# Kernel optimization log

Measured on AMD Instinct MI355X. Metric: run time of the kernel, lower is better.

The kernel has to match this reference:

```python
import jax, jax.numpy as jnp
import numpy as np

N = 1024        # hidden_size
M = 16000       # output_size (vocab)
T = 50          # encoder sequence length
NP = 50         # max_length (attention proj dim n_prime)


def setup_inputs() -> dict:
    key = jax.random.key(0)
    ks = jax.random.split(key, 24)
    f32 = jnp.float32
    def rnd(k, shape):
        return jax.random.normal(k, shape, dtype=f32) * 0.02
    inp = {
        'output': jax.random.normal(ks[0], (M, 1), dtype=f32),
        'hidden': jax.random.normal(ks[1], (N, 1), dtype=f32),
        'encoder_outputs': jax.random.normal(ks[2], (T, 2 * N), dtype=f32),
        # decoder GRU-like weights
        'W':  rnd(ks[3], (M, N)),
        'Wz': rnd(ks[4], (M, N)),
        'Wr': rnd(ks[5], (M, N)),
        'Wo': rnd(ks[6], (M, 2 * N)),
        'U':  rnd(ks[7], (N, N)),
        'Uz': rnd(ks[8], (N, N)),
        'Ur': rnd(ks[9], (N, N)),
        'Uo': rnd(ks[10], (4 * N, N)),
        'C':  rnd(ks[11], (2 * N, N)),
        'Cz': rnd(ks[12], (2 * N, N)),
        'Cr': rnd(ks[13], (2 * N, N)),
        'Co': rnd(ks[14], (4 * N, 2 * N)),
        'Vo': rnd(ks[15], (4 * N, M)),
        # attention weights
        'Va': rnd(ks[16], (NP, 1)),
        'Wa': rnd(ks[17], (NP, N)),
        'Ua': rnd(ks[18], (NP, 2 * N)),
    }
    return inp


def reference(output, hidden, encoder_outputs, W, Wz, Wr, Wo, U, Uz, Ur, Uo,
              C, Cz, Cr, Co, Vo, Va, Wa, Ua):
    y, s, h = output, hidden, encoder_outputs  # (M,1), (N,1), (T,2N)
    # --- Bahdanau attention (vectorized version of get_c's python loop) ---
    # e_i = exp(Va^T tanh(Wa@s + Ua@h_i)); then normalized -> softmax
    scores = jnp.tanh((Wa @ s).T + h @ Ua.T) @ Va          # (T,1)
    attn = jax.nn.softmax(scores[:, 0])                     # (T,)
    alpha = h * attn[:, None]                               # (T,2N) weighted enc outputs
    c = jnp.sum(alpha, axis=0)[:, None]                     # (2N,1) context
    # --- GRU-like decoder step (note: s_tilde uses sigmoid, per source) ---
    r = jax.nn.sigmoid(Wr.T @ y + Ur.T @ s + Cr.T @ c)      # (N,1)
    z = jax.nn.sigmoid(Wz.T @ y + Uz.T @ s + Cz.T @ c)      # (N,1)
    s_tilde = jax.nn.sigmoid(W.T @ y + U.T @ (r * s) + C.T @ c)
    s_new = (1.0 - z) * s + z * s_tilde                     # (N,1)
    # --- maxout output layer ---
    t_tilde = jax.nn.sigmoid(Uo @ s_new + Vo @ y + Co @ c)  # (4N,1)
    t = jnp.max(t_tilde.reshape(-1, 2, 1), axis=1)          # (2N,1) pairwise max
    logits = Wo @ t                                         # (M,1)
    log_sm = jax.nn.log_softmax(logits, axis=0)             # log(softmax(., dim=0))
    # dropout in the source is applied to a discarded value -> mathematical no-op
    return (log_sm, s_new, alpha)
```

## Files before the change

kernel.cpp:

```cpp
#include <hip/hip_runtime.h>
#include <math.h>

#define DEV_INLINE __device__ __forceinline__

DEV_INLINE float sigmoidf_(float x) { return 1.0f / (1.0f + expf(-x)); }

DEV_INLINE float wave_reduce(float v) {
#pragma unroll
    for (int off = 32; off; off >>= 1) v += __shfl_down(v, off, 64);
    return v;
}

DEV_INLINE float wave_dotN(const float* __restrict__ row, const float* __restrict__ x,
                           int nv, int lane) {
    const float4* r4 = (const float4*)row;
    const float4* x4 = (const float4*)x;
    float a0 = 0.f, a1 = 0.f, a2 = 0.f, a3 = 0.f;
    int i = lane;
    for (; i + 192 < nv; i += 256) {
        float4 p0 = r4[i],       q0 = x4[i];
        float4 p1 = r4[i + 64],  q1 = x4[i + 64];
        float4 p2 = r4[i + 128], q2 = x4[i + 128];
        float4 p3 = r4[i + 192], q3 = x4[i + 192];
        a0 = fmaf(p0.x, q0.x, fmaf(p0.y, q0.y, fmaf(p0.z, q0.z, fmaf(p0.w, q0.w, a0))));
        a1 = fmaf(p1.x, q1.x, fmaf(p1.y, q1.y, fmaf(p1.z, q1.z, fmaf(p1.w, q1.w, a1))));
        a2 = fmaf(p2.x, q2.x, fmaf(p2.y, q2.y, fmaf(p2.z, q2.z, fmaf(p2.w, q2.w, a2))));
        a3 = fmaf(p3.x, q3.x, fmaf(p3.y, q3.y, fmaf(p3.z, q3.z, fmaf(p3.w, q3.w, a3))));
    }
    for (; i < nv; i += 64) {
        float4 p = r4[i], q = x4[i];
        a0 = fmaf(p.x, q.x, fmaf(p.y, q.y, fmaf(p.z, q.z, fmaf(p.w, q.w, a0))));
    }
    return wave_reduce(a0 + a1 + a2 + a3);
}

DEV_INLINE void colgemv_block(const float* __restrict__ A, const float* __restrict__ x,
                              float* __restrict__ out, int r0, int r1) {
    int c4 = threadIdx.x;
    const float4* A4 = (const float4*)A;
    float4 s0 = make_float4(0.f, 0.f, 0.f, 0.f);
    float4 s1 = make_float4(0.f, 0.f, 0.f, 0.f);
    int r = r0;
    for (; r + 8 <= r1; r += 8) {
        float4 av[8];
        float xs[8];
#pragma unroll
        for (int k = 0; k < 8; ++k) av[k] = A4[(size_t)(r + k) * 256 + c4];
#pragma unroll
        for (int k = 0; k < 8; ++k) xs[k] = x[r + k];
#pragma unroll
        for (int k = 0; k < 8; ++k) {
            float4 a = av[k];
            float xv = xs[k];
            if (k & 1) {
                s1.x = fmaf(xv, a.x, s1.x); s1.y = fmaf(xv, a.y, s1.y);
                s1.z = fmaf(xv, a.z, s1.z); s1.w = fmaf(xv, a.w, s1.w);
            } else {
                s0.x = fmaf(xv, a.x, s0.x); s0.y = fmaf(xv, a.y, s0.y);
                s0.z = fmaf(xv, a.z, s0.z); s0.w = fmaf(xv, a.w, s0.w);
            }
        }
    }
    for (; r < r1; ++r) {
        float xv = x[r];
        float4 a = A4[(size_t)r * 256 + c4];
        s0.x = fmaf(xv, a.x, s0.x); s0.y = fmaf(xv, a.y, s0.y);
        s0.z = fmaf(xv, a.z, s0.z); s0.w = fmaf(xv, a.w, s0.w);
    }
    int c = c4 * 4;
    atomicAdd(out + c + 0, s0.x + s1.x);
    atomicAdd(out + c + 1, s0.y + s1.y);
    atomicAdd(out + c + 2, s0.z + s1.z);
    atomicAdd(out + c + 3, s0.w + s1.w);
}

__global__ void k_scores(const float* __restrict__ Wa, const float* __restrict__ Ua,
                         const float* __restrict__ h, const float* __restrict__ s,
                         float* __restrict__ em) {
    int i = blockIdx.x;
    int w = threadIdx.x >> 6, lane = threadIdx.x & 63;
    for (int j = w; j < 50; j += 4) {
        float d1 = wave_dotN(Wa + j * 1024, s, 256, lane);
        float d2 = wave_dotN(Ua + j * 2048, h + i * 2048, 512, lane);
        if (lane == 0) em[i * 50 + j] = tanhf(d1 + d2);
    }
}

__global__ void k_alpha_c(const float* __restrict__ h, const float* __restrict__ Va,
                          const float* __restrict__ em, float* __restrict__ cvec,
                          float* __restrict__ alpha_out) {
    __shared__ float attn_s[50];
    int tid = threadIdx.x;
    if (tid < 64) {
        float sc = -1e30f;
        if (tid < 50) {
            float t = 0.f;
            for (int j = 0; j < 50; ++j) t = fmaf(Va[j], em[tid * 50 + j], t);
            sc = t;
        }
        float m = sc;
#pragma unroll
        for (int off = 32; off; off >>= 1) m = fmaxf(m, __shfl_xor(m, off, 64));
        float e = (tid < 50) ? expf(sc - m) : 0.f;
        float ssum = e;
#pragma unroll
        for (int off = 32; off; off >>= 1) ssum += __shfl_xor(ssum, off, 64);
        if (tid < 50) attn_s[tid] = e / ssum;
    }
    __syncthreads();
    int g = blockIdx.x * 256 + tid;
    float csum = 0.f;
    for (int i = 0; i < 50; ++i) {
        float a = h[i * 2048 + g] * attn_s[i];
        alpha_out[i * 2048 + g] = a;
        csum += a;
    }
    cvec[g] = csum;
}

__global__ void k_megaA(const float* __restrict__ W, const float* __restrict__ Wz,
                        const float* __restrict__ Wr, const float* __restrict__ Uz,
                        const float* __restrict__ Ur, const float* __restrict__ C,
                        const float* __restrict__ Cz, const float* __restrict__ Cr,
                        const float* __restrict__ Vo, const float* __restrict__ Co,
                        const float* __restrict__ y, const float* __restrict__ s,
                        const float* __restrict__ cvec, float* acc_r, float* acc_z,
                        float* acc_st, float* acc_t) {
    int b = blockIdx.x;
    if (b < 128) { colgemv_block(W, y, acc_st, b * 125, b * 125 + 125); return; }
    b -= 128;
    if (b < 128) { colgemv_block(Wz, y, acc_z, b * 125, b * 125 + 125); return; }
    b -= 128;
    if (b < 128) { colgemv_block(Wr, y, acc_r, b * 125, b * 125 + 125); return; }
    b -= 128;
    if (b < 8) { colgemv_block(Uz, s, acc_z, b * 128, b * 128 + 128); return; }
    b -= 8;
    if (b < 8) { colgemv_block(Ur, s, acc_r, b * 128, b * 128 + 128); return; }
    b -= 8;
    if (b < 16) { colgemv_block(C, cvec, acc_st, b * 128, b * 128 + 128); return; }
    b -= 16;
    if (b < 16) { colgemv_block(Cz, cvec, acc_z, b * 128, b * 128 + 128); return; }
    b -= 16;
    if (b < 16) { colgemv_block(Cr, cvec, acc_r, b * 128, b * 128 + 128); return; }
    b -= 16;
    {
        int wid = (b * 256 + threadIdx.x) >> 6;
        int lane = threadIdx.x & 63;
        float v1 = wave_dotN(Vo + (size_t)wid * 16000, y, 4000, lane);
        float v2 = wave_dotN(Co + (size_t)wid * 2048, cvec, 512, lane);
        if (lane == 0) acc_t[wid] = v1 + v2;
    }
}

__global__ void k_rzUst(const float* __restrict__ U, const float* __restrict__ acc_r,
                        const float* __restrict__ s, float* acc_st) {
    __shared__ float rs_s[1024];
    int tid = threadIdx.x;
#pragma unroll
    for (int k = 0; k < 4; ++k) {
        int n = tid + 256 * k;
        rs_s[n] = sigmoidf_(acc_r[n]) * s[n];
    }
    __syncthreads();
    colgemv_block(U, rs_s, acc_st, blockIdx.x * 128, blockIdx.x * 128 + 128);
}

__global__ void k_uoco_snew(const float* __restrict__ Uo, const float* __restrict__ acc_st,
                            const float* __restrict__ acc_z, const float* __restrict__ s,
                            float* __restrict__ acc_t, float* __restrict__ out_snew) {
    __shared__ float sn[1024];
    int tid = threadIdx.x;
#pragma unroll
    for (int k = 0; k < 4; ++k) {
        int n = tid + 256 * k;
        float z = sigmoidf_(acc_z[n]);
        float st = sigmoidf_(acc_st[n]);
        float v = (1.f - z) * s[n] + z * st;
        sn[n] = v;
        if (blockIdx.x == 0) out_snew[n] = v;
    }
    __syncthreads();
    int w = tid >> 6, lane = tid & 63;
#pragma unroll
    for (int k = 0; k < 4; ++k) {
        int row = blockIdx.x * 16 + w * 4 + k;
        float d = wave_dotN(Uo + (size_t)row * 1024, sn, 256, lane);
        if (lane == 0) acc_t[row] += d;
    }
}

__global__ void k_tmax(const float* __restrict__ acc_t, float* __restrict__ tvec) {
    int k = blockIdx.x * 256 + threadIdx.x;
    tvec[k] = fmaxf(sigmoidf_(acc_t[2 * k]), sigmoidf_(acc_t[2 * k + 1]));
}

__global__ void k_wo(const float* __restrict__ Wo, const float* __restrict__ tvec,
                     float* __restrict__ logits) {
    int wid = (blockIdx.x * 256 + threadIdx.x) >> 6;
    int lane = threadIdx.x & 63;
    float v = wave_dotN(Wo + (size_t)wid * 2048, tvec, 512, lane);
    if (lane == 0) logits[wid] = v;
}

__global__ void k_logsm(float* __restrict__ out) {
    __shared__ float red[16];
    __shared__ float bval;
    int tid = threadIdx.x, lane = tid & 63, w = tid >> 6;
    float m = -1e30f;
    for (int i = tid; i < 16000; i += 1024) m = fmaxf(m, out[i]);
#pragma unroll
    for (int off = 32; off; off >>= 1) m = fmaxf(m, __shfl_xor(m, off, 64));
    if (lane == 0) red[w] = m;
    __syncthreads();
    if (tid == 0) {
        float mm = red[0];
        for (int i = 1; i < 16; ++i) mm = fmaxf(mm, red[i]);
        bval = mm;
    }
    __syncthreads();
    float M = bval;
    float sum = 0.f;
    for (int i = tid; i < 16000; i += 1024) sum += expf(out[i] - M);
#pragma unroll
    for (int off = 32; off; off >>= 1) sum += __shfl_xor(sum, off, 64);
    if (lane == 0) red[w] = sum;
    __syncthreads();
    if (tid == 0) {
        float ss = 0.f;
        for (int i = 0; i < 16; ++i) ss += red[i];
        bval = M + logf(ss);
    }
    __syncthreads();
    float lse = bval;
    for (int i = tid; i < 16000; i += 1024) out[i] -= lse;
}

extern "C" void kernel_launch(void* const* d_in, const int* in_sizes, int n_in,
                              void* d_out, int out_size, void* d_ws, size_t ws_size,
                              hipStream_t stream) {
    const float* y  = (const float*)d_in[0];
    const float* s  = (const float*)d_in[1];
    const float* h  = (const float*)d_in[2];
    const float* W  = (const float*)d_in[3];
    const float* Wz = (const float*)d_in[4];
    const float* Wr = (const float*)d_in[5];
    const float* Wo = (const float*)d_in[6];
    const float* U  = (const float*)d_in[7];
    const float* Uz = (const float*)d_in[8];
    const float* Ur = (const float*)d_in[9];
    const float* Uo = (const float*)d_in[10];
    const float* C  = (const float*)d_in[11];
    const float* Cz = (const float*)d_in[12];
    const float* Cr = (const float*)d_in[13];
    const float* Co = (const float*)d_in[14];
    const float* Vo = (const float*)d_in[15];
    const float* Va = (const float*)d_in[16];
    const float* Wa = (const float*)d_in[17];
    const float* Ua = (const float*)d_in[18];

    float* out = (float*)d_out;
    float* ws  = (float*)d_ws;

    float* acc_r  = ws;
    float* acc_z  = ws + 1024;
    float* acc_st = ws + 2048;
    float* acc_t  = ws + 3072;
    float* em     = ws + 7168;
    float* cvec   = ws + 9728;
    float* tvec   = ws + 11776;

    hipMemsetAsync(ws, 0, 3072 * sizeof(float), stream);
    k_scores<<<50, 256, 0, stream>>>(Wa, Ua, h, s, em);
    k_alpha_c<<<8, 256, 0, stream>>>(h, Va, em, cvec, out + 17024);
    k_megaA<<<1472, 256, 0, stream>>>(W, Wz, Wr, Uz, Ur, C, Cz, Cr, Vo, Co,
                                      y, s, cvec, acc_r, acc_z, acc_st, acc_t);
    k_rzUst<<<8, 256, 0, stream>>>(U, acc_r, s, acc_st);
    k_uoco_snew<<<256, 256, 0, stream>>>(Uo, acc_st, acc_z, s, acc_t, out + 16000);
    k_tmax<<<8, 256, 0, stream>>>(acc_t, tvec);
    k_wo<<<4000, 256, 0, stream>>>(Wo, tvec, out);
    k_logsm<<<1, 1024, 0, stream>>>(out);
}
```

Measured before the change: 685.5 us.

## Fuse all decoder stages into one persistent kernel with atomic flag dependencies

Replaces the eight kernel launches with a single 1835-block kernel in which block ranges play each stage and use global atomic counters to wait for their producer stages. Independent work such as the Vo/W/Wz/Wr GEMVs can overlap the attention and later stages, and launch gaps and the separate tmax and logsoftmax kernels go away; the maxout is folded into the Uo stage and log-softmax is vectorized. The cost is spin-waiting blocks occupying CUs. Correctness relies on blocks being scheduled in roughly ascending order, so there is a deadlock risk if consumers become resident before producers.

After: 1.133 ms. 65.3% more time.

```diff
diff --git a/kernel.cpp b/kernel.cpp
--- a/kernel.cpp
+++ b/kernel.cpp
@@ -74,165 +74,203 @@
     atomicAdd(out + c + 3, s0.w + s1.w);
 }
 
-__global__ void k_scores(const float* __restrict__ Wa, const float* __restrict__ Ua,
-                         const float* __restrict__ h, const float* __restrict__ s,
-                         float* __restrict__ em) {
-    int i = blockIdx.x;
-    int w = threadIdx.x >> 6, lane = threadIdx.x & 63;
-    for (int j = w; j < 50; j += 4) {
-        float d1 = wave_dotN(Wa + j * 1024, s, 256, lane);
-        float d2 = wave_dotN(Ua + j * 2048, h + i * 2048, 512, lane);
-        if (lane == 0) em[i * 50 + j] = tanhf(d1 + d2);
-    }
-}
-
-__global__ void k_alpha_c(const float* __restrict__ h, const float* __restrict__ Va,
-                          const float* __restrict__ em, float* __restrict__ cvec,
-                          float* __restrict__ alpha_out) {
-    __shared__ float attn_s[50];
-    int tid = threadIdx.x;
-    if (tid < 64) {
-        float sc = -1e30f;
-        if (tid < 50) {
-            float t = 0.f;
-            for (int j = 0; j < 50; ++j) t = fmaf(Va[j], em[tid * 50 + j], t);
-            sc = t;
-        }
-        float m = sc;
+DEV_INLINE void signal_flag(int* f) {
+    __threadfence();
+    __syncthreads();
+    if (threadIdx.x == 0) atomicAdd(f, 1);
+}
+DEV_INLINE void wait_flag(int* f, int target) {
+    if (threadIdx.x == 0) {
+        while (atomicAdd(f, 0) < target) __builtin_amdgcn_s_sleep(127);
+    }
+    __syncthreads();
+    __threadfence();
+}
+
+__global__ __launch_bounds__(256, 8) void k_fused(
+    const float* __restrict__ y, const float* __restrict__ s, const float* __restrict__ h,
+    const float* __restrict__ W, const float* __restrict__ Wz, const float* __restrict__ Wr,
+    const float* __restrict__ Wo, const float* __restrict__ U, const float* __restrict__ Uz,
+    const float* __restrict__ Ur, const float* __restrict__ Uo, const float* __restrict__ C,
+    const float* __restrict__ Cz, const float* __restrict__ Cr, const float* __restrict__ Co,
+    const float* __restrict__ Vo, const float* __restrict__ Va, const float* __restrict__ Wa,
+    const float* __restrict__ Ua, float* __restrict__ out, float* __restrict__ ws)
+{
+    float* acc_r  = ws;
+    float* acc_z  = ws + 1024;
+    float* acc_st = ws + 2048;
+    float* acc_t  = ws + 3072;
+    int*   flags  = (int*)(ws + 7168);
+    float* em     = ws + 7296;
+    float* cvec   = ws + 9856;
+    float* tvec   = ws + 11904;
+    int* fSC  = flags;
+    int* fAL  = flags + 16;
+    int* fR   = flags + 32;
+    int* fMID = flags + 48;
+    int* fU   = flags + 64;
+    int* fWO  = flags + 80;
+
+    __shared__ float sm[1024];
+    __shared__ float sred[8];
+    __shared__ float sbval;
+
+    const int bid  = blockIdx.x;
+    const int tid  = threadIdx.x;
+    const int w    = tid >> 6;
+    const int lane = tid & 63;
+
+    if (bid < 50) {
+        int i = bid;
+        for (int j = w; j < 50; j += 4) {
+            float d1 = wave_dotN(Wa + j * 1024, s, 256, lane);
+            float d2 = wave_dotN(Ua + j * 2048, h + i * 2048, 512, lane);
+            if (lane == 0) em[i * 50 + j] = tanhf(d1 + d2);
+        }
+        signal_flag(fSC);
+        return;
+    }
+    if (bid < 58) {
+        wait_flag(fSC, 50);
+        if (tid < 64) {
+            float sc = -1e30f;
+            if (tid < 50) {
+                float t = 0.f;
+                for (int j = 0; j < 50; ++j) t = fmaf(Va[j], em[tid * 50 + j], t);
+                sc = t;
+            }
+            float m = sc;
+#pragma unroll
+            for (int off = 32; off; off >>= 1) m = fmaxf(m, __shfl_xor(m, off, 64));
+            float e = (tid < 50) ? expf(sc - m) : 0.f;
+            float ssum = e;
+#pragma unroll
+            for (int off = 32; off; off >>= 1) ssum += __shfl_xor(ssum, off, 64);
+            if (tid < 50) sm[tid] = e / ssum;
+        }
+        __syncthreads();
+        int g = (bid - 50) * 256 + tid;
+        float csum = 0.f;
+        float* alpha_out = out + 17024;
+        for (int i2 = 0; i2 < 50; ++i2) {
+            float a = h[i2 * 2048 + g] * sm[i2];
+            alpha_out[i2 * 2048 + g] = a;
+            csum += a;
+        }
+        cvec[g] = csum;
+        signal_flag(fAL);
+        return;
+    }
+    if (bid < 186) { int b = bid - 58;  colgemv_block(W,  y, acc_st, b * 125, b * 125 + 125); signal_flag(fMID); return; }
+    if (bid < 314) { int b = bid - 186; colgemv_block(Wz, y, acc_z,  b * 125, b * 125 + 125); signal_flag(fMID); return; }
+    if (bid < 442) { int b = bid - 314; colgemv_block(Wr, y, acc_r,  b * 125, b * 125 + 125); signal_flag(fR);   return; }
+    if (bid < 450) { int b = bid - 442; colgemv_block(Uz, s, acc_z,  b * 128, b * 128 + 128); signal_flag(fMID); return; }
+    if (bid < 458) { int b = bid - 450; colgemv_block(Ur, s, acc_r,  b * 128, b * 128 + 128); signal_flag(fR);   return; }
+    if (bid < 474) { int b = bid - 458; wait_flag(fAL, 8); colgemv_block(C,  cvec, acc_st, b * 128, b * 128 + 128); signal_flag(fMID); return; }
+    if (bid < 490) { int b = bid - 474; wait_flag(fAL, 8); colgemv_block(Cz, cvec, acc_z,  b * 128, b * 128 + 128); signal_flag(fMID); return; }
+    if (bid < 506) { int b = bid - 490; wait_flag(fAL, 8); colgemv_block(Cr, cvec, acc_r,  b * 128, b * 128 + 128); signal_flag(fR);   return; }
+    if (bid < 522) {
+        int b = bid - 506;
+        wait_flag(fR, 152);
+#pragma unroll
+        for (int k = 0; k < 4; ++k) {
+            int n = tid + 256 * k;
+            sm[n] = sigmoidf_(acc_r[n]) * s[n];
+        }
+        __syncthreads();
+        colgemv_block(U, sm, acc_st, b * 64, b * 64 + 64);
+        signal_flag(fMID);
+        return;
+    }
+    if (bid < 778) {
+        int b = bid - 522;
+        int row0 = b * 16 + w * 4;
+        float v1[4];
+#pragma unroll
+        for (int k = 0; k < 4; ++k)
+            v1[k] = wave_dotN(Vo + (size_t)(row0 + k) * 16000, y, 4000, lane);
+        wait_flag(fAL, 8);
+#pragma unroll
+        for (int k = 0; k < 4; ++k) {
+            float v2 = wave_dotN(Co + (size_t)(row0 + k) * 2048, cvec, 512, lane);
+            if (lane == 0) atomicAdd(acc_t + row0 + k, v1[k] + v2);
+        }
+        signal_flag(fMID);
+        return;
+    }
+    if (bid < 1034) {
+        int b = bid - 778;
+        wait_flag(fMID, 568);
+#pragma unroll
+        for (int k = 0; k < 4; ++k) {
+            int n = tid + 256 * k;
+            float z  = sigmoidf_(acc_z[n]);
+            float st = sigmoidf_(acc_st[n]);
+            float v = (1.f - z) * s[n] + z * st;
+            sm[n] = v;
+            if (b == 0) out[16000 + n] = v;
+        }
+        __syncthreads();
+        float m0 = 0.f;
+#pragma unroll
+        for (int k = 0; k < 4; ++k) {
+            int row = b * 16 + w * 4 + k;
+            float d = wave_dotN(Uo + (size_t)row * 1024, sm, 256, lane);
+            if (lane == 0) {
+                float tf = sigmoidf_(acc_t[row] + d);
+                if (k & 1) tvec[row >> 1] = fmaxf(m0, tf);
+                else       m0 = tf;
+            }
+        }
+        signal_flag(fU);
+        return;
+    }
+    if (bid < 1834) {
+        int b = bid - 1034;
+        wait_flag(fU, 256);
+        int gw = b * 4 + w;
+#pragma unroll
+        for (int k = 0; k < 5; ++k) {
+            int row = gw * 5 + k;
+            float v = wave_dotN(Wo + (size_t)row * 2048, tvec, 512, lane);
+            if (lane == 0) out[row] = v;
+        }
+        signal_flag(fWO);
+        return;
+    }
+    wait_flag(fWO, 800);
+    {
+        float4* o4 = (float4*)out;
+        float m = -1e30f;
+        for (int i = tid; i < 4000; i += 256) {
+            float4 v = o4[i];
+            m = fmaxf(m, fmaxf(fmaxf(v.x, v.y), fmaxf(v.z, v.w)));
+        }
 #pragma unroll
         for (int off = 32; off; off >>= 1) m = fmaxf(m, __shfl_xor(m, off, 64));
-        float e = (tid < 50) ? expf(sc - m) : 0.f;
-        float ssum = e;
-#pragma unroll
-        for (int off = 32; off; off >>= 1) ssum += __shfl_xor(ssum, off, 64);
-        if (tid < 50) attn_s[tid] = e / ssum;
-    }
-    __syncthreads();
-    int g = blockIdx.x * 256 + tid;
-    float csum = 0.f;
-    for (int i = 0; i < 50; ++i) {
-        float a = h[i * 2048 + g] * attn_s[i];
-        alpha_out[i * 2048 + g] = a;
-        csum += a;
-    }
-    cvec[g] = csum;
-}
-
-__global__ void k_megaA(const float* __restrict__ W, const float* __restrict__ Wz,
-                        const float* __restrict__ Wr, const float* __restrict__ Uz,
-                        const float* __restrict__ Ur, const float* __restrict__ C,
-                        const float* __restrict__ Cz, const float* __restrict__ Cr,
-                        const float* __restrict__ Vo, const float* __restrict__ Co,
-                        const float* __restrict__ y, const float* __restrict__ s,
-                        const float* __restrict__ cvec, float* acc_r, float* acc_z,
-                        float* acc_st, float* acc_t) {
-    int b = blockIdx.x;
-    if (b < 128) { colgemv_block(W, y, acc_st, b * 125, b * 125 + 125); return; }
-    b -= 128;
-    if (b < 128) { colgemv_block(Wz, y, acc_z, b * 125, b * 125 + 125); return; }
-    b -= 128;
-    if (b < 128) { colgemv_block(Wr, y, acc_r, b * 125, b * 125 + 125); return; }
-    b -= 128;
-    if (b < 8) { colgemv_block(Uz, s, acc_z, b * 128, b * 128 + 128); return; }
-    b -= 8;
-    if (b < 8) { colgemv_block(Ur, s, acc_r, b * 128, b * 128 + 128); return; }
-    b -= 8;
-    if (b < 16) { colgemv_block(C, cvec, acc_st, b * 128, b * 128 + 128); return; }
-    b -= 16;
-    if (b < 16) { colgemv_block(Cz, cvec, acc_z, b * 128, b * 128 + 128); return; }
-    b -= 16;
-    if (b < 16) { colgemv_block(Cr, cvec, acc_r, b * 128, b * 128 + 128); return; }
-    b -= 16;
-    {
-        int wid = (b * 256 + threadIdx.x) >> 6;
-        int lane = threadIdx.x & 63;
-        float v1 = wave_dotN(Vo + (size_t)wid * 16000, y, 4000, lane);
-        float v2 = wave_dotN(Co + (size_t)wid * 2048, cvec, 512, lane);
-        if (lane == 0) acc_t[wid] = v1 + v2;
-    }
-}
-
-__global__ void k_rzUst(const float* __restrict__ U, const float* __restrict__ acc_r,
-                        const float* __restrict__ s, float* acc_st) {
-    __shared__ float rs_s[1024];
-    int tid = threadIdx.x;
-#pragma unroll
-    for (int k = 0; k < 4; ++k) {
-        int n = tid + 256 * k;
-        rs_s[n] = sigmoidf_(acc_r[n]) * s[n];
-    }
-    __syncthreads();
-    colgemv_block(U, rs_s, acc_st, blockIdx.x * 128, blockIdx.x * 128 + 128);
-}
-
-__global__ void k_uoco_snew(const float* __restrict__ Uo, const float* __restrict__ acc_st,
-                            const float* __restrict__ acc_z, const float* __restrict__ s,
-                            float* __restrict__ acc_t, float* __restrict__ out_snew) {
-    __shared__ float sn[1024];
-    int tid = threadIdx.x;
-#pragma unroll
-    for (int k = 0; k < 4; ++k) {
-        int n = tid + 256 * k;
-        float z = sigmoidf_(acc_z[n]);
-        float st = sigmoidf_(acc_st[n]);
-        float v = (1.f - z) * s[n] + z * st;
-        sn[n] = v;
-        if (blockIdx.x == 0) out_snew[n] = v;
-    }
-    __syncthreads();
-    int w = tid >> 6, lane = tid & 63;
-#pragma unroll
-    for (int k = 0; k < 4; ++k) {
-        int row = blockIdx.x * 16 + w * 4 + k;
-        float d = wave_dotN(Uo + (size_t)row * 1024, sn, 256, lane);
-        if (lane == 0) acc_t[row] += d;
-    }
-}
-
-__global__ void k_tmax(const float* __restrict__ acc_t, float* __restrict__ tvec) {
-    int k = blockIdx.x * 256 + threadIdx.x;
-    tvec[k] = fmaxf(sigmoidf_(acc_t[2 * k]), sigmoidf_(acc_t[2 * k + 1]));
-}
-
-__global__ void k_wo(const float* __restrict__ Wo, const float* __restrict__ tvec,
-                     float* __restrict__ logits) {
-    int wid = (blockIdx.x * 256 + threadIdx.x) >> 6;
-    int lane = threadIdx.x & 63;
-    float v = wave_dotN(Wo + (size_t)wid * 2048, tvec, 512, lane);
-    if (lane == 0) logits[wid] = v;
-}
-
-__global__ void k_logsm(float* __restrict__ out) {
-    __shared__ float red[16];
-    __shared__ float bval;
-    int tid = threadIdx.x, lane = tid & 63, w = tid >> 6;
-    float m = -1e30f;
-    for (int i = tid; i < 16000; i += 1024) m = fmaxf(m, out[i]);
-#pragma unroll
-    for (int off = 32; off; off >>= 1) m = fmaxf(m, __shfl_xor(m, off, 64));
-    if (lane == 0) red[w] = m;
-    __syncthreads();
-    if (tid == 0) {
-        float mm = red[0];
-        for (int i = 1; i < 16; ++i) mm = fmaxf(mm, red[i]);
-        bval = mm;
-    }
-    __syncthreads();
-    float M = bval;
-    float sum = 0.f;
-    for (int i = tid; i < 16000; i += 1024) sum += expf(out[i] - M);
-#pragma unroll
-    for (int off = 32; off; off >>= 1) sum += __shfl_xor(sum, off, 64);
-    if (lane == 0) red[w] = sum;
-    __syncthreads();
-    if (tid == 0) {
-        float ss = 0.f;
-        for (int i = 0; i < 16; ++i) ss += red[i];
-        bval = M + logf(ss);
-    }
-    __syncthreads();
-    float lse = bval;
-    for (int i = tid; i < 16000; i += 1024) out[i] -= lse;
+        if (lane == 0) sred[w] = m;
+        __syncthreads();
+        if (tid == 0) sbval = fmaxf(fmaxf(sred[0], sred[1]), fmaxf(sred[2], sred[3]));
+        __syncthreads();
+        float M = sbval;
+        float sum = 0.f;
+        for (int i = tid; i < 4000; i += 256) {
+            float4 v = o4[i];
+            sum += expf(v.x - M) + expf(v.y - M) + expf(v.z - M) + expf(v.w - M);
+        }
+#pragma unroll
+        for (int off = 32; off; off >>= 1) sum += __shfl_xor(sum, off, 64);
+        if (lane == 0) sred[w] = sum;
+        __syncthreads();
+        if (tid == 0) sbval = M + logf(sred[0] + sred[1] + sred[2] + sred[3]);
+        __syncthreads();
+        float lse = sbval;
+        for (int i = tid; i < 4000; i += 256) {
+            float4 v = o4[i];
+            v.x -= lse; v.y -= lse; v.z -= lse; v.w -= lse;
+            o4[i] = v;
+        }
+    }
 }
 
 extern "C" void kernel_launch(void* const* d_in, const int* in_sizes, int n_in,
@@ -261,22 +299,7 @@
     float* out = (float*)d_out;
     float* ws  = (float*)d_ws;
 
-    float* acc_r  = ws;
-    float* acc_z  = ws + 1024;
-    float* acc_st = ws + 2048;
-    float* acc_t  = ws + 3072;
-    float* em     = ws + 7168;
-    float* cvec   = ws + 9728;
-    float* tvec   = ws + 11776;
-
-    hipMemsetAsync(ws, 0, 3072 * sizeof(float), stream);
-    k_scores<<<50, 256, 0, stream>>>(Wa, Ua, h, s, em);
-    k_alpha_c<<<8, 256, 0, stream>>>(h, Va, em, cvec, out + 17024);
-    k_megaA<<<1472, 256, 0, stream>>>(W, Wz, Wr, Uz, Ur, C, Cz, Cr, Vo, Co,
-                                      y, s, cvec, acc_r, acc_z, acc_st, acc_t);
-    k_rzUst<<<8, 256, 0, stream>>>(U, acc_r, s, acc_st);
-    k_uoco_snew<<<256, 256, 0, stream>>>(Uo, acc_st, acc_z, s, acc_t, out + 16000);
-    k_tmax<<<8, 256, 0, stream>>>(acc_t, tvec);
-    k_wo<<<4000, 256, 0, stream>>>(Wo, tvec, out);
-    k_logsm<<<1, 1024, 0, stream>>>(out);
-}
+    hipMemsetAsync(ws, 0, 7296 * sizeof(float), stream);
+    k_fused<<<1835, 256, 0, stream>>>(y, s, h, W, Wz, Wr, Wo, U, Uz, Ur, Uo,
+                                      C, Cz, Cr, Co, Vo, Va, Wa, Ua, out, ws);
+}
```
